# Kernel tuning notes

Hardware: AMD Instinct MI355X
Metric: run time of the kernel (lower is better)

## Reference

```python
import jax, jax.numpy as jnp
import numpy as np

DIM = 100
SAMPLE = 12
NEG = -9e15
LRELU = 0.2  # opt.alpha


def _forward(emb, pos_table, w1, w2, glu1_w, glu2_w, glu2_b,
             a0, a1, a2, a3, gw1, gw2, gw3, num_w, mask_item,
             alias_inputs, adj, items, seq_features, adj_all):
    B, L = items.shape
    h = emb[items]  # [B, L, D]

    # ---- LocalAggregator: e_k[b,i,j] = leaky_relu(sum_d h[b,i,d]*h[b,j,d]*a_k[d])
    # (same math as tiling to [B, N*N, D] then matmul with a_k, without the huge intermediate)
    def rel(a):
        return jax.nn.leaky_relu(jnp.einsum('bid,bjd->bij', h, h * a[:, 0]), LRELU)

    alpha = jnp.full((B, L, L), NEG, dtype=h.dtype)
    for k, a in enumerate((a0, a1, a2, a3)):
        alpha = jnp.where(adj == k + 1, rel(a), alpha)
    alpha = jax.nn.softmax(alpha, axis=-1)
    h_local = jnp.einsum('bij,bjd->bid', alpha, h)

    # ---- Global: sample 1-hop neighbors from adj_all / num tables
    nbr_idx = adj_all[items]          # [B, L, S]
    nbr_w = num_w[items]              # [B, L, S]
    nbr_vec = emb[nbr_idx]            # [B, L, S, D]

    # session info (mean of masked seq-feature embeddings)
    item_emb = emb[seq_features] * mask_item[..., None]
    sess = jnp.sum(item_emb, axis=1) / jnp.sum(mask_item, axis=-1, keepdims=True)  # [B, D]
    sess = jnp.broadcast_to(sess[:, None, :], (B, L, DIM))

    # GlobalAggregator with extra_vector
    a_in = jnp.concatenate([sess[:, :, None, :] * nbr_vec, nbr_w[..., None]], axis=-1)  # [B,L,S,D+1]
    att = jax.nn.leaky_relu(a_in @ gw1, LRELU)          # [B, L, S, D]
    att = jax.nn.softmax((att @ gw2)[..., 0], axis=-1)  # [B, L, S]
    agg = jnp.sum(att[..., None] * nbr_vec, axis=-2)    # [B, L, D]
    h_global = jax.nn.relu(jnp.concatenate([h, agg], axis=-1) @ gw3)

    h_comb = h_local + h_global
    seq_hidden = jnp.take_along_axis(h_comb, alias_inputs[..., None], axis=1)  # [B, L, D]

    rmask = mask_item[..., None]
    pos = jnp.broadcast_to(pos_table[:L][None], seq_hidden.shape)
    hs = jnp.sum(seq_hidden * rmask, axis=1) / jnp.sum(rmask, axis=1)  # [B, D]
    nh = jnp.tanh(jnp.concatenate([pos, seq_hidden], axis=-1) @ w1)
    nh = jax.nn.sigmoid(nh @ glu1_w + (hs @ glu2_w + glu2_b)[:, None, :])
    beta = (nh @ w2) * rmask                 # [B, L, 1]
    select = jnp.sum(beta * seq_hidden, 1)   # [B, D]
    score = select @ emb[1:].T               # skip item id 0 (padding)
    return jax.nn.softmax(score, axis=-1)


def setup_inputs():
    key = jax.random.key(0)
    B, L, NN, S, D = 256, 64, 100000, SAMPLE, DIM
    stdv = 1.0 / np.sqrt(D)
    ks = jax.random.split(key, 24)
    u = lambda k, s: jax.random.uniform(k, s, jnp.float32, -stdv, stdv)
    return {
        'emb': u(ks[0], (NN, D)),
        'pos_table': u(ks[1], (200, D)),
        'w1': u(ks[2], (2 * D, D)),
        'w2': u(ks[3], (D, 1)),
        'glu1_w': u(ks[4], (D, D)),
        'glu2_w': u(ks[5], (D, D)),
        'glu2_b': u(ks[6], (D,)),
        'a0': u(ks[7], (D, 1)),
        'a1': u(ks[8], (D, 1)),
        'a2': u(ks[9], (D, 1)),
        'a3': u(ks[10], (D, 1)),
        'gw1': u(ks[11], (D + 1, D)),
        'gw2': u(ks[12], (D, 1)),
        'gw3': u(ks[13], (2 * D, D)),
        'num_w': jax.random.uniform(ks[14], (NN, S), jnp.float32, 0.0, 1.0),
        'mask_item': jnp.ones((B, L), jnp.float32),
        'alias_inputs': jax.random.randint(ks[15], (B, L), 0, L),
        'adj': jax.random.randint(ks[16], (B, L, L), 0, 5),
        'items': jax.random.randint(ks[17], (B, L), 0, NN),
        'seq_features': jax.random.randint(ks[18], (B, L), 0, NN),
        'adj_all': jax.random.randint(ks[19], (NN, S), 0, NN),
    }


def reference(emb, pos_table, w1, w2, glu1_w, glu2_w, glu2_b, a0, a1, a2, a3,
              gw1, gw2, gw3, num_w, mask_item, alias_inputs, adj, items,
              seq_features, adj_all):
    return _forward(emb, pos_table, w1, w2, glu1_w, glu2_w, glu2_b,
                    a0, a1, a2, a3, gw1, gw2, gw3, num_w, mask_item,
                    alias_inputs, adj, items, seq_features, adj_all)
```

## Files before the change

kernel.cpp:

```cpp
#include <hip/hip_runtime.h>
#include <math.h>

#define B 256
#define L 64
#define D 100
#define S 12
#define NN 100000
#define E 99999
#define NEG -9e15f
#define LRELU 0.2f
#define M3A (B*L*S)
#define NT5 782

__device__ __forceinline__ float lrelu(float x){ return x > 0.f ? x : LRELU*x; }

__global__ void k0_pos(const float* __restrict__ pos, const float* __restrict__ w1,
                       float* __restrict__ pos_part){
    int l = blockIdx.x; int d = threadIdx.x;
    if (d >= D) return;
    float acc = 0.f;
    for (int c = 0; c < D; ++c) acc += pos[l*D+c] * w1[c*D+d];
    pos_part[l*D+d] = acc;
}

__global__ void k1_gather(const float* __restrict__ emb, const int* __restrict__ items,
                          const int* __restrict__ seqf, const float* __restrict__ mask,
                          float* __restrict__ h, float* __restrict__ sess){
    int b = blockIdx.x; int tid = threadIdx.x;
    for (int t = tid; t < L*D; t += blockDim.x){
        int l = t / D, d = t % D;
        h[(b*L+l)*D + d] = emb[(long)items[b*L+l]*D + d];
    }
    if (tid < D){
        float acc = 0.f, msum = 0.f;
        for (int l = 0; l < L; ++l){
            float mk = mask[b*L+l];
            acc  += emb[(long)seqf[b*L+l]*D + tid] * mk;
            msum += mk;
        }
        sess[b*D+tid] = acc / msum;
    }
}

__global__ __launch_bounds__(256) void k2_local(const float* __restrict__ h,
                         const int* __restrict__ adj,
                         const float* __restrict__ a0, const float* __restrict__ a1,
                         const float* __restrict__ a2, const float* __restrict__ a3,
                         float* __restrict__ hcomb){
    __shared__ __align__(16) float Hd[L*132];
    __shared__ float Alr[L*66];
    __shared__ __align__(16) float a4s[D*4];
    int tid = threadIdx.x;
    int tx = tid & 15, ty = tid >> 4;
    int b = blockIdx.x;

    for (int t = tid; t < D; t += 256){
        a4s[t*4+0] = a0[t]; a4s[t*4+1] = a1[t]; a4s[t*4+2] = a2[t]; a4s[t*4+3] = a3[t];
    }
    for (int e = tid; e < L*D; e += 256){
        int i = e / D, d = e - i*D;
        Hd[i*132 + d] = h[(long)(b*L+i)*D + d];
    }
    for (int e = tid; e < L*32; e += 256){
        int i = e >> 5, c = D + (e & 31);
        Hd[i*132 + c] = 0.f;
    }
    __syncthreads();

    int ksel[4][4];
    #pragma unroll
    for (int i=0;i<4;++i)
        #pragma unroll
        for (int j=0;j<4;++j)
            ksel[i][j] = adj[((long)b*L + ty*4+i)*L + tx*4+j];

    float e0[4][4]={}, e1[4][4]={}, e2[4][4]={}, e3[4][4]={};
    for (int d = 0; d < D; ++d){
        float4 aw = *(const float4*)&a4s[d*4];
        float hi[4], hj[4];
        #pragma unroll
        for (int i=0;i<4;++i) hi[i] = Hd[(ty*4+i)*132 + d];
        #pragma unroll
        for (int j=0;j<4;++j) hj[j] = Hd[(tx*4+j)*132 + d];
        #pragma unroll
        for (int i=0;i<4;++i)
            #pragma unroll
            for (int j=0;j<4;++j){
                float p = hi[i]*hj[j];
                e0[i][j] += p*aw.x;
                e1[i][j] += p*aw.y;
                e2[i][j] += p*aw.z;
                e3[i][j] += p*aw.w;
            }
    }

    #pragma unroll
    for (int i=0;i<4;++i){
        float s[4];
        #pragma unroll
        for (int j=0;j<4;++j){
            int k = ksel[i][j];
            float ev = (k==1) ? e0[i][j] : (k==2) ? e1[i][j]
                     : (k==3) ? e2[i][j] : e3[i][j];
            s[j] = (k>=1 && k<=4) ? lrelu(ev) : NEG;
        }
        float m = fmaxf(fmaxf(s[0],s[1]), fmaxf(s[2],s[3]));
        #pragma unroll
        for (int off=1; off<16; off<<=1) m = fmaxf(m, __shfl_xor(m, off));
        float es[4], sum = 0.f;
        #pragma unroll
        for (int j=0;j<4;++j){ es[j] = expf(s[j]-m); sum += es[j]; }
        #pragma unroll
        for (int off=1; off<16; off<<=1) sum += __shfl_xor(sum, off);
        float inv = 1.f/sum;
        #pragma unroll
        for (int j=0;j<4;++j) Alr[(ty*4+i)*66 + tx*4+j] = es[j]*inv;
    }
    __syncthreads();

    float o[4][8];
    #pragma unroll
    for (int i=0;i<4;++i)
        #pragma unroll
        for (int jj=0;jj<8;++jj) o[i][jj] = 0.f;
    for (int j = 0; j < L; ++j){
        float al[4];
        #pragma unroll
        for (int i=0;i<4;++i) al[i] = Alr[(ty*4+i)*66 + j];
        float4 b0 = *(const float4*)&Hd[j*132 + tx*4];
        float4 b1 = *(const float4*)&Hd[j*132 + 64 + tx*4];
        float bv[8] = {b0.x,b0.y,b0.z,b0.w,b1.x,b1.y,b1.z,b1.w};
        #pragma unroll
        for (int i=0;i<4;++i)
            #pragma unroll
            for (int jj=0;jj<8;++jj) o[i][jj] += al[i]*bv[jj];
    }
    #pragma unroll
    for (int i=0;i<4;++i){
        int row = ty*4+i;
        #pragma unroll
        for (int jj=0;jj<8;++jj){
            int d = (jj<4) ? (tx*4+jj) : (64 + tx*4 + (jj-4));
            if (d < D) hcomb[(long)(b*L+row)*D + d] = o[i][jj];
        }
    }
}

__global__ __launch_bounds__(256) void k3a_logits(const float* __restrict__ emb,
                          const float* __restrict__ sess,
                          const int* __restrict__ items, const int* __restrict__ adj_all,
                          const float* __restrict__ num_w,
                          const float* __restrict__ gw1, const float* __restrict__ gw2,
                          float* __restrict__ att_l){
    __shared__ __align__(16) float As[52*64];
    __shared__ __align__(16) float Bs[52*128];
    __shared__ float ss[104];
    __shared__ int   idxr[64];
    __shared__ float nbwr[64];
    __shared__ float gw2l[128];
    int tid = threadIdx.x;
    int tx = tid & 15, ty = tid >> 4;
    int r0 = blockIdx.x * 64;
    int b  = r0 / (L*S);

    if (tid < 64){
        int r = r0 + tid;
        int bl = r / S, s = r - bl*S;
        int it = items[bl];
        idxr[tid] = adj_all[it*S + s];
        nbwr[tid] = num_w[it*S + s];
    }
    if (tid < 104) ss[tid] = (tid < D) ? sess[b*D + tid] : 0.f;
    if (tid < 128) gw2l[tid] = (tid < D) ? gw2[tid] : 0.f;
    __syncthreads();

    float acc[4][8];
    #pragma unroll
    for (int i=0;i<4;++i)
        #pragma unroll
        for (int j=0;j<8;++j) acc[i][j] = 0.f;

    for (int chunk = 0; chunk < 2; ++chunk){
        int c0 = chunk*52;
        for (int e = tid; e < 64*13; e += 256){
            int rl = e & 63, cq = e >> 6;
            int cb = c0 + cq*4;
            float vx=0.f, vy=0.f, vz=0.f, vw=0.f;
            if (cb < D){
                const float4 v = *(const float4*)&emb[(long)idxr[rl]*D + cb];
                vx = v.x*ss[cb]; vy = v.y*ss[cb+1]; vz = v.z*ss[cb+2]; vw = v.w*ss[cb+3];
            } else if (cb == D){
                vx = nbwr[rl];
            }
            As[(cq*4+0)*64 + rl] = vx;
            As[(cq*4+1)*64 + rl] = vy;
            As[(cq*4+2)*64 + rl] = vz;
            As[(cq*4+3)*64 + rl] = vw;
        }
        for (int e = tid; e < 52*128; e += 256){
            int d = e & 127, cc = e >> 7;
            int c = c0 + cc;
            Bs[cc*128 + d] = (c <= D && d < D) ? gw1[c*D + d] : 0.f;
        }
        __syncthreads();
        for (int k = 0; k < 52; ++k){
            float4 a  = *(const float4*)&As[k*64 + ty*4];
            float4 b0 = *(const float4*)&Bs[k*128 + tx*4];
            float4 b1 = *(const float4*)&Bs[k*128 + 64 + tx*4];
            float av[4] = {a.x,a.y,a.z,a.w};
            float bv[8] = {b0.x,b0.y,b0.z,b0.w,b1.x,b1.y,b1.z,b1.w};
            #pragma unroll
            for (int i=0;i<4;++i)
                #pragma unroll
                for (int j=0;j<8;++j) acc[i][j] += av[i]*bv[j];
        }
        __syncthreads();
    }
    float g[8];
    #pragma unroll
    for (int j=0;j<8;++j) g[j] = gw2l[(j<4) ? (tx*4+j) : (64 + tx*4 + (j-4))];
    #pragma unroll
    for (int i=0;i<4;++i){
        float p = 0.f;
        #pragma unroll
        for (int j=0;j<8;++j) p += lrelu(acc[i][j]) * g[j];
        #pragma unroll
        for (int off=1; off<16; off<<=1) p += __shfl_xor(p, off);
        if (tx == 0) att_l[r0 + ty*4 + i] = p;
    }
}

__global__ __launch_bounds__(256) void k3b_agg(const float* __restrict__ emb,
                          const int* __restrict__ items, const int* __restrict__ adj_all,
                          const float* __restrict__ att_l,
                          float* __restrict__ agg){
    int p = blockIdx.x*2 + (threadIdx.x >> 7);
    int t = threadIdx.x & 127;
    float lg[S];
    float m = -INFINITY;
    #pragma unroll
    for (int s=0;s<S;++s){ lg[s] = att_l[p*S + s]; m = fmaxf(m, lg[s]); }
    float sum = 0.f;
    #pragma unroll
    for (int s=0;s<S;++s){ lg[s] = expf(lg[s]-m); sum += lg[s]; }
    float inv = 1.f/sum;
    if (t < D){
        int it = items[p];
        float acc = 0.f;
        #pragma unroll
        for (int s=0;s<S;++s){
            int idx = adj_all[it*S + s];
            acc += lg[s]*inv * emb[(long)idx*D + t];
        }
        agg[p*D + t] = acc;
    }
}

__global__ __launch_bounds__(256) void k3c_hg(const float* __restrict__ h,
                          const float* __restrict__ agg, const float* __restrict__ gw3,
                          float* __restrict__ hcomb){
    __shared__ __align__(16) float As[52*64];
    __shared__ __align__(16) float Bs[52*128];
    int tid = threadIdx.x;
    int tx = tid & 15, ty = tid >> 4;
    int r0 = blockIdx.x * 64;

    float acc[4][8];
    #pragma unroll
    for (int i=0;i<4;++i)
        #pragma unroll
        for (int j=0;j<8;++j) acc[i][j] = 0.f;

    for (int chunk = 0; chunk < 4; ++chunk){
        int c0 = chunk*52;
        for (int e = tid; e < 64*13; e += 256){
            int rl = e & 63, cq = e >> 6;
            int cb = c0 + cq*4;
            float4 v = {0.f,0.f,0.f,0.f};
            if (cb < D)            v = *(const float4*)&h[(long)(r0+rl)*D + cb];
            else if (cb < 2*D)     v = *(const float4*)&agg[(long)(r0+rl)*D + (cb-D)];
            As[(cq*4+0)*64 + rl] = v.x;
            As[(cq*4+1)*64 + rl] = v.y;
            As[(cq*4+2)*64 + rl] = v.z;
            As[(cq*4+3)*64 + rl] = v.w;
        }
        for (int e = tid; e < 52*128; e += 256){
            int d = e & 127, cc = e >> 7;
            int c = c0 + cc;
            Bs[cc*128 + d] = (c < 2*D && d < D) ? gw3[c*D + d] : 0.f;
        }
        __syncthreads();
        for (int k = 0; k < 52; ++k){
            float4 a  = *(const float4*)&As[k*64 + ty*4];
            float4 b0 = *(const float4*)&Bs[k*128 + tx*4];
            float4 b1 = *(const float4*)&Bs[k*128 + 64 + tx*4];
            float av[4] = {a.x,a.y,a.z,a.w};
            float bv[8] = {b0.x,b0.y,b0.z,b0.w,b1.x,b1.y,b1.z,b1.w};
            #pragma unroll
            for (int i=0;i<4;++i)
                #pragma unroll
                for (int j=0;j<8;++j) acc[i][j] += av[i]*bv[j];
        }
        __syncthreads();
    }
    #pragma unroll
    for (int i=0;i<4;++i){
        int r = r0 + ty*4 + i;
        #pragma unroll
        for (int j=0;j<8;++j){
            int d = (j<4) ? (tx*4+j) : (64 + tx*4 + (j-4));
            if (d < D){
                long o = (long)r*D + d;
                hcomb[o] += fmaxf(acc[i][j], 0.f);
            }
        }
    }
}

__global__ __launch_bounds__(128) void k4a_gate(const float* __restrict__ hcomb,
                          const int* __restrict__ alias_in, const float* __restrict__ mask,
                          const float* __restrict__ glu2_w, const float* __restrict__ glu2_b,
                          float* __restrict__ gate){
    int b = blockIdx.x; int tid = threadIdx.x;
    __shared__ float hsl[D];
    __shared__ float mkl[L];
    __shared__ int   al[L];
    if (tid < L){ al[tid] = alias_in[b*L+tid]; mkl[tid] = mask[b*L+tid]; }
    __syncthreads();
    if (tid < D){
        float acc = 0.f, msum = 0.f;
        for (int l = 0; l < L; ++l){
            acc  += hcomb[(long)(b*L + al[l])*D + tid] * mkl[l];
            msum += mkl[l];
        }
        hsl[tid] = acc / msum;
    }
    __syncthreads();
    if (tid < D){
        float g = glu2_b[tid];
        for (int c = 0; c < D; ++c) g += hsl[c]*glu2_w[c*D+tid];
        gate[b*D+tid] = g;
    }
}

__global__ __launch_bounds__(256) void k4b_nh1(const float* __restrict__ hcomb,
                          const int* __restrict__ alias_in,
                          const float* __restrict__ w1, const float* __restrict__ pos_part,
                          float* __restrict__ nh1){
    __shared__ __align__(16) float As[52*64];
    __shared__ __align__(16) float Bs[52*128];
    __shared__ int al[64];
    int tid = threadIdx.x;
    int tx = tid & 15, ty = tid >> 4;
    int b = blockIdx.x;
    int r0 = b * 64;

    if (tid < 64) al[tid] = alias_in[r0 + tid];
    __syncthreads();

    float acc[4][8];
    #pragma unroll
    for (int i=0;i<4;++i)
        #pragma unroll
        for (int j=0;j<8;++j) acc[i][j] = 0.f;

    for (int chunk = 0; chunk < 2; ++chunk){
        int c0 = chunk*52;
        for (int e = tid; e < 64*13; e += 256){
            int rl = e & 63, cq = e >> 6;
            int cb = c0 + cq*4;
            float4 v = {0.f,0.f,0.f,0.f};
            if (cb < D) v = *(const float4*)&hcomb[(long)(r0 + al[rl])*D + cb];
            As[(cq*4+0)*64 + rl] = v.x;
            As[(cq*4+1)*64 + rl] = v.y;
            As[(cq*4+2)*64 + rl] = v.z;
            As[(cq*4+3)*64 + rl] = v.w;
        }
        for (int e = tid; e < 52*128; e += 256){
            int d = e & 127, cc = e >> 7;
            int c = c0 + cc;
            Bs[cc*128 + d] = (c < D && d < D) ? w1[(D+c)*D + d] : 0.f;
        }
        __syncthreads();
        for (int k = 0; k < 52; ++k){
            float4 a  = *(const float4*)&As[k*64 + ty*4];
            float4 b0 = *(const float4*)&Bs[k*128 + tx*4];
            float4 b1 = *(const float4*)&Bs[k*128 + 64 + tx*4];
            float av[4] = {a.x,a.y,a.z,a.w};
            float bv[8] = {b0.x,b0.y,b0.z,b0.w,b1.x,b1.y,b1.z,b1.w};
            #pragma unroll
            for (int i=0;i<4;++i)
                #pragma unroll
                for (int j=0;j<8;++j) acc[i][j] += av[i]*bv[j];
        }
        __syncthreads();
    }
    #pragma unroll
    for (int i=0;i<4;++i){
        int rl = ty*4 + i;
        #pragma unroll
        for (int j=0;j<8;++j){
            int d = (j<4) ? (tx*4+j) : (64 + tx*4 + (j-4));
            if (d < D){
                float v = tanhf(acc[i][j] + pos_part[rl*D + d]);
                nh1[(long)(r0+rl)*D + d] = v;
            }
        }
    }
}

__global__ __launch_bounds__(256) void k4c_select(const float* __restrict__ nh1,
                          const float* __restrict__ hcomb, const int* __restrict__ alias_in,
                          const float* __restrict__ glu1_w, const float* __restrict__ gate,
                          const float* __restrict__ w2, const float* __restrict__ mask,
                          float* __restrict__ sel_out){
    __shared__ __align__(16) float As[104*64];
    __shared__ __align__(16) float Bs[52*128];
    __shared__ __align__(16) float Ss[64*D];
    __shared__ float red[16*128];
    __shared__ float w2l[128];
    __shared__ float mkl[64];
    __shared__ int   al[64];
    int tid = threadIdx.x;
    int tx = tid & 15, ty = tid >> 4;
    int b = blockIdx.x;
    int r0 = b * 64;

    if (tid < 64){ al[tid] = alias_in[r0 + tid]; mkl[tid] = mask[r0 + tid]; }
    if (tid < 128) w2l[tid] = (tid < D) ? w2[tid] : 0.f;
    __syncthreads();

    for (int e = tid; e < 64*26; e += 256){
        int rl = e & 63, cq = e >> 6;
        int cb = cq*4;
        float4 v = {0.f,0.f,0.f,0.f};
        if (cb < D) v = *(const float4*)&nh1[(long)(r0+rl)*D + cb];
        As[(cb+0)*64 + rl] = v.x;
        As[(cb+1)*64 + rl] = v.y;
        As[(cb+2)*64 + rl] = v.z;
        As[(cb+3)*64 + rl] = v.w;
    }
    for (int e = tid; e < 64*25; e += 256){
        int rl = e / 25, q = e % 25;
        *(float4*)&Ss[rl*D + q*4] = *(const float4*)&hcomb[(long)(r0 + al[rl])*D + q*4];
    }

    float acc[4][8];
    #pragma unroll
    for (int i=0;i<4;++i)
        #pragma unroll
        for (int j=0;j<8;++j) acc[i][j] = 0.f;

    for (int chunk = 0; chunk < 2; ++chunk){
        int c0 = chunk*52;
        __syncthreads();
        for (int e = tid; e < 52*128; e += 256){
            int d = e & 127, cc = e >> 7;
            int c = c0 + cc;
            Bs[cc*128 + d] = (c < D && d < D) ? glu1_w[c*D + d] : 0.f;
        }
        __syncthreads();
        for (int k = 0; k < 52; ++k){
            float4 a  = *(const float4*)&As[(c0+k)*64 + ty*4];
            float4 b0 = *(const float4*)&Bs[k*128 + tx*4];
            float4 b1 = *(const float4*)&Bs[k*128 + 64 + tx*4];
            float av[4] = {a.x,a.y,a.z,a.w};
            float bv[8] = {b0.x,b0.y,b0.z,b0.w,b1.x,b1.y,b1.z,b1.w};
            #pragma unroll
            for (int i=0;i<4;++i)
                #pragma unroll
                for (int j=0;j<8;++j) acc[i][j] += av[i]*bv[j];
        }
    }
    __syncthreads();

    float gl[8];
    #pragma unroll
    for (int j=0;j<8;++j){
        int d = (j<4) ? (tx*4+j) : (64 + tx*4 + (j-4));
        gl[j] = (d < D) ? gate[b*D + d] : 0.f;
    }
    float sp[8];
    #pragma unroll
    for (int j=0;j<8;++j) sp[j] = 0.f;
    #pragma unroll
    for (int i=0;i<4;++i){
        int rl = ty*4 + i;
        float p = 0.f;
        #pragma unroll
        for (int j=0;j<8;++j){
            int d = (j<4) ? (tx*4+j) : (64 + tx*4 + (j-4));
            float z = acc[i][j] + gl[j];
            float nh2 = 1.f/(1.f+expf(-z));
            p += nh2 * w2l[d];
        }
        #pragma unroll
        for (int off=1; off<16; off<<=1) p += __shfl_xor(p, off);
        float beta = p * mkl[rl];
        #pragma unroll
        for (int j=0;j<8;++j){
            int d = (j<4) ? (tx*4+j) : (64 + tx*4 + (j-4));
            if (d < D) sp[j] += beta * Ss[rl*D + d];
        }
    }
    #pragma unroll
    for (int j=0;j<8;++j){
        int d = (j<4) ? (tx*4+j) : (64 + tx*4 + (j-4));
        red[ty*128 + d] = sp[j];
    }
    __syncthreads();
    if (tid < 128){
        float s = 0.f;
        #pragma unroll
        for (int g=0; g<16; ++g) s += red[g*128 + tid];
        if (tid < D) sel_out[b*D + tid] = s;
    }
}

__global__ __launch_bounds__(256) void k5_score(const float* __restrict__ emb,
                                                const float* __restrict__ sel,
                                                float* __restrict__ out,
                                                float* __restrict__ pstats){
    __shared__ __align__(16) float As[52*64];
    __shared__ __align__(16) float Bs[52*128];
    int tid = threadIdx.x;
    int tx = tid & 15, ty = tid >> 4;
    int n0 = blockIdx.x * 128;
    int m0 = blockIdx.y * 64;

    float acc[4][8];
    #pragma unroll
    for (int i=0;i<4;++i)
        #pragma unroll
        for (int j=0;j<8;++j) acc[i][j] = 0.f;

    for (int chunk = 0; chunk < 2; ++chunk){
        int c0 = chunk*52;
        for (int e = tid; e < 64*13; e += 256){
            int rl = e & 63, cq = e >> 6;
            int cb = c0 + cq*4;
            float4 v = {0.f,0.f,0.f,0.f};
            if (cb < D) v = *(const float4*)&sel[(long)(m0+rl)*D + cb];
            As[(cq*4+0)*64 + rl] = v.x;
            As[(cq*4+1)*64 + rl] = v.y;
            As[(cq*4+2)*64 + rl] = v.z;
            As[(cq*4+3)*64 + rl] = v.w;
        }
        for (int e = tid; e < 128*13; e += 256){
            int nl = e & 127, cq = e >> 7;
            int cb = c0 + cq*4;
            int n = n0 + nl;
            float4 v = {0.f,0.f,0.f,0.f};
            if (cb < D && n < E) v = *(const float4*)&emb[(long)(1+n)*D + cb];
            Bs[(cq*4+0)*128 + nl] = v.x;
            Bs[(cq*4+1)*128 + nl] = v.y;
            Bs[(cq*4+2)*128 + nl] = v.z;
            Bs[(cq*4+3)*128 + nl] = v.w;
        }
        __syncthreads();
        for (int k = 0; k < 52; ++k){
            float4 a  = *(const float4*)&As[k*64 + ty*4];
            float4 b0 = *(const float4*)&Bs[k*128 + tx*4];
            float4 b1 = *(const float4*)&Bs[k*128 + 64 + tx*4];
            float av[4] = {a.x,a.y,a.z,a.w};
            float bv[8] = {b0.x,b0.y,b0.z,b0.w,b1.x,b1.y,b1.z,b1.w};
            #pragma unroll
            for (int i=0;i<4;++i)
                #pragma unroll
                for (int j=0;j<8;++j) acc[i][j] += av[i]*bv[j];
        }
        __syncthreads();
    }
    bool fullTile = (n0 + 128 <= E);
    #pragma unroll
    for (int i=0;i<4;++i){
        int m = m0 + ty*4 + i;
        long rowo = (long)m*E;
        if (fullTile){
            *(float4*)&out[rowo + n0 + tx*4]      = *(float4*)&acc[i][0];
            *(float4*)&out[rowo + n0 + 64 + tx*4] = *(float4*)&acc[i][4];
        } else {
            #pragma unroll
            for (int j=0;j<8;++j){
                int n = n0 + ((j<4) ? (tx*4+j) : (64 + tx*4 + (j-4)));
                if (n < E) out[rowo + n] = acc[i][j];
            }
        }
        float mx = -INFINITY, sm = 0.f;
        #pragma unroll
        for (int j=0;j<8;++j){
            int n = n0 + ((j<4) ? (tx*4+j) : (64 + tx*4 + (j-4)));
            if (n < E){
                float v = acc[i][j];
                if (v > mx){ sm = sm*expf(mx - v) + 1.f; mx = v; }
                else         sm += expf(v - mx);
            }
        }
        #pragma unroll
        for (int off=1; off<16; off<<=1){
            float mo = __shfl_xor(mx, off);
            float so = __shfl_xor(sm, off);
            float mm = fmaxf(mx, mo);
            float sn = 0.f;
            if (mx > -INFINITY) sn += sm*expf(mx-mm);
            if (mo > -INFINITY) sn += so*expf(mo-mm);
            mx = mm; sm = sn;
        }
        if (tx == 0){
            long o = ((long)m*NT5 + blockIdx.x)*2;
            pstats[o] = mx; pstats[o+1] = sm;
        }
    }
}

__global__ __launch_bounds__(256) void k7_combine(const float* __restrict__ pstats,
                                                  float* __restrict__ MS){
    int row = blockIdx.x;
    int tid = threadIdx.x;
    float m = -INFINITY, s = 0.f;
    for (int t = tid; t < NT5; t += 256){
        long o = ((long)row*NT5 + t)*2;
        float m2 = pstats[o], s2 = pstats[o+1];
        float mm = fmaxf(m, m2);
        float sn = 0.f;
        if (m  > -INFINITY) sn += s *expf(m -mm);
        if (m2 > -INFINITY) sn += s2*expf(m2-mm);
        m = mm; s = sn;
    }
    __shared__ float ms[256], ss[256];
    ms[tid] = m; ss[tid] = s;
    __syncthreads();
    for (int off = 128; off >= 1; off >>= 1){
        if (tid < off){
            float m1 = ms[tid], s1 = ss[tid];
            float m2 = ms[tid+off], s2 = ss[tid+off];
            float mm = fmaxf(m1, m2);
            float sn = 0.f;
            if (m1 > -INFINITY) sn += s1*expf(m1-mm);
            if (m2 > -INFINITY) sn += s2*expf(m2-mm);
            ms[tid] = mm; ss[tid] = sn;
        }
        __syncthreads();
    }
    if (tid == 0){ MS[row*2] = ms[0]; MS[row*2+1] = 1.f/ss[0]; }
}

__global__ __launch_bounds__(256) void k8_norm(float* __restrict__ out,
                                               const float* __restrict__ MS){
    int b = blockIdx.y;
    int n = blockIdx.x*256 + threadIdx.x;
    if (n < E){
        float m = MS[b*2], invs = MS[b*2+1];
        long i = (long)b*E + n;
        out[i] = expf(out[i] - m) * invs;
    }
}

extern "C" void kernel_launch(void* const* d_in, const int* in_sizes, int n_in,
                              void* d_out, int out_size, void* d_ws, size_t ws_size,
                              hipStream_t stream) {
    const float* emb       = (const float*)d_in[0];
    const float* pos_table = (const float*)d_in[1];
    const float* w1        = (const float*)d_in[2];
    const float* w2        = (const float*)d_in[3];
    const float* glu1_w    = (const float*)d_in[4];
    const float* glu2_w    = (const float*)d_in[5];
    const float* glu2_b    = (const float*)d_in[6];
    const float* a0        = (const float*)d_in[7];
    const float* a1        = (const float*)d_in[8];
    const float* a2        = (const float*)d_in[9];
    const float* a3        = (const float*)d_in[10];
    const float* gw1       = (const float*)d_in[11];
    const float* gw2       = (const float*)d_in[12];
    const float* gw3       = (const float*)d_in[13];
    const float* num_w     = (const float*)d_in[14];
    const float* mask      = (const float*)d_in[15];
    const int*   alias_in  = (const int*)d_in[16];
    const int*   adj       = (const int*)d_in[17];
    const int*   items     = (const int*)d_in[18];
    const int*   seqf      = (const int*)d_in[19];
    const int*   adj_all   = (const int*)d_in[20];

    float* ws       = (float*)d_ws;
    float* h        = ws;
    float* hcomb    = h + B*L*D;
    float* sess     = hcomb + B*L*D;
    float* pos_part = sess + B*D;
    float* sel      = pos_part + L*D;
    float* att_l    = sel + B*D;
    float* agg      = att_l + M3A;
    float* pstats   = agg + B*L*D;
    float* MS       = pstats + B*NT5*2;
    float* gate     = MS + B*2;
    float* nh1      = agg;

    float* out = (float*)d_out;

    k0_pos    <<<dim3(L), dim3(128), 0, stream>>>(pos_table, w1, pos_part);
    k1_gather <<<dim3(B), dim3(128), 0, stream>>>(emb, items, seqf, mask, h, sess);
    k2_local  <<<dim3(B), dim3(256), 0, stream>>>(h, adj, a0, a1, a2, a3, hcomb);
    k3a_logits<<<dim3(M3A/64), dim3(256), 0, stream>>>(emb, sess, items, adj_all, num_w,
                                                       gw1, gw2, att_l);
    k3b_agg   <<<dim3(B*L/2), dim3(256), 0, stream>>>(emb, items, adj_all, att_l, agg);
    k3c_hg    <<<dim3(B*L/64), dim3(256), 0, stream>>>(h, agg, gw3, hcomb);
    k4a_gate  <<<dim3(B), dim3(128), 0, stream>>>(hcomb, alias_in, mask, glu2_w, glu2_b, gate);
    k4b_nh1   <<<dim3(B), dim3(256), 0, stream>>>(hcomb, alias_in, w1, pos_part, nh1);
    k4c_select<<<dim3(B), dim3(256), 0, stream>>>(nh1, hcomb, alias_in, glu1_w, gate,
                                                  w2, mask, sel);
    k5_score  <<<dim3(NT5, 4), dim3(256), 0, stream>>>(emb, sel, out, pstats);
    k7_combine<<<dim3(B), dim3(256), 0, stream>>>(pstats, MS);
    k8_norm   <<<dim3((E + 255)/256, B), dim3(256), 0, stream>>>(out, MS);
}
```

Measured before the change: 665.9 us.

## Enlarge GEMM row tiles to 128 and vectorize gather and normalize kernels

The score GEMM and the neighbor-logit GEMM now compute 128-row tiles with an 8x8 per-thread accumulator instead of 64-row tiles. This halves the number of times the embedding table and gw1 are re-read from memory. The embedding gather in k1 and the softmax normalization in k8 now use float4 loads and stores, and k8 runs over a flat 1D grid. In exchange, register pressure and shared memory per block rise, which may lower occupancy, and k3a now reloads items, adj_all and sess from global memory inside its staging loop.

Result: faster. 642.8 us (-3.5%).

```diff
diff --git a/kernel.cpp b/kernel.cpp
--- a/kernel.cpp
+++ b/kernel.cpp
@@ -27,9 +27,10 @@
                           const int* __restrict__ seqf, const float* __restrict__ mask,
                           float* __restrict__ h, float* __restrict__ sess){
     int b = blockIdx.x; int tid = threadIdx.x;
-    for (int t = tid; t < L*D; t += blockDim.x){
-        int l = t / D, d = t % D;
-        h[(b*L+l)*D + d] = emb[(long)items[b*L+l]*D + d];
+    for (int e = tid; e < L*25; e += blockDim.x){
+        int l = e / 25, q = e % 25;
+        *(float4*)&h[(long)(b*L+l)*D + q*4] =
+            *(const float4*)&emb[(long)items[b*L+l]*D + q*4];
     }
     if (tid < D){
         float acc = 0.f, msum = 0.f;
@@ -152,50 +153,40 @@
                           const float* __restrict__ num_w,
                           const float* __restrict__ gw1, const float* __restrict__ gw2,
                           float* __restrict__ att_l){
-    __shared__ __align__(16) float As[52*64];
+    __shared__ __align__(16) float As[52*128];
     __shared__ __align__(16) float Bs[52*128];
-    __shared__ float ss[104];
-    __shared__ int   idxr[64];
-    __shared__ float nbwr[64];
-    __shared__ float gw2l[128];
     int tid = threadIdx.x;
     int tx = tid & 15, ty = tid >> 4;
-    int r0 = blockIdx.x * 64;
+    int r0 = blockIdx.x * 128;
     int b  = r0 / (L*S);
 
-    if (tid < 64){
-        int r = r0 + tid;
-        int bl = r / S, s = r - bl*S;
-        int it = items[bl];
-        idxr[tid] = adj_all[it*S + s];
-        nbwr[tid] = num_w[it*S + s];
-    }
-    if (tid < 104) ss[tid] = (tid < D) ? sess[b*D + tid] : 0.f;
-    if (tid < 128) gw2l[tid] = (tid < D) ? gw2[tid] : 0.f;
-    __syncthreads();
-
-    float acc[4][8];
-    #pragma unroll
-    for (int i=0;i<4;++i)
+    float acc[8][8];
+    #pragma unroll
+    for (int i=0;i<8;++i)
         #pragma unroll
         for (int j=0;j<8;++j) acc[i][j] = 0.f;
 
     for (int chunk = 0; chunk < 2; ++chunk){
         int c0 = chunk*52;
-        for (int e = tid; e < 64*13; e += 256){
-            int rl = e & 63, cq = e >> 6;
+        for (int e = tid; e < 128*13; e += 256){
+            int rl = e & 127, cq = e >> 7;
             int cb = c0 + cq*4;
+            int r = r0 + rl;
+            int bl = r / S, s = r - bl*S;
+            int it = items[bl];
             float vx=0.f, vy=0.f, vz=0.f, vw=0.f;
             if (cb < D){
-                const float4 v = *(const float4*)&emb[(long)idxr[rl]*D + cb];
-                vx = v.x*ss[cb]; vy = v.y*ss[cb+1]; vz = v.z*ss[cb+2]; vw = v.w*ss[cb+3];
+                int idx = adj_all[it*S + s];
+                const float4 v  = *(const float4*)&emb[(long)idx*D + cb];
+                const float4 sv = *(const float4*)&sess[(long)b*D + cb];
+                vx = v.x*sv.x; vy = v.y*sv.y; vz = v.z*sv.z; vw = v.w*sv.w;
             } else if (cb == D){
-                vx = nbwr[rl];
+                vx = num_w[it*S + s];
             }
-            As[(cq*4+0)*64 + rl] = vx;
-            As[(cq*4+1)*64 + rl] = vy;
-            As[(cq*4+2)*64 + rl] = vz;
-            As[(cq*4+3)*64 + rl] = vw;
+            As[(cq*4+0)*128 + rl] = vx;
+            As[(cq*4+1)*128 + rl] = vy;
+            As[(cq*4+2)*128 + rl] = vz;
+            As[(cq*4+3)*128 + rl] = vw;
         }
         for (int e = tid; e < 52*128; e += 256){
             int d = e & 127, cc = e >> 7;
@@ -204,13 +195,14 @@
         }
         __syncthreads();
         for (int k = 0; k < 52; ++k){
-            float4 a  = *(const float4*)&As[k*64 + ty*4];
+            float4 a0v = *(const float4*)&As[k*128 + ty*8];
+            float4 a1v = *(const float4*)&As[k*128 + ty*8 + 4];
             float4 b0 = *(const float4*)&Bs[k*128 + tx*4];
             float4 b1 = *(const float4*)&Bs[k*128 + 64 + tx*4];
-            float av[4] = {a.x,a.y,a.z,a.w};
+            float av[8] = {a0v.x,a0v.y,a0v.z,a0v.w,a1v.x,a1v.y,a1v.z,a1v.w};
             float bv[8] = {b0.x,b0.y,b0.z,b0.w,b1.x,b1.y,b1.z,b1.w};
             #pragma unroll
-            for (int i=0;i<4;++i)
+            for (int i=0;i<8;++i)
                 #pragma unroll
                 for (int j=0;j<8;++j) acc[i][j] += av[i]*bv[j];
         }
@@ -218,15 +210,18 @@
     }
     float g[8];
     #pragma unroll
-    for (int j=0;j<8;++j) g[j] = gw2l[(j<4) ? (tx*4+j) : (64 + tx*4 + (j-4))];
-    #pragma unroll
-    for (int i=0;i<4;++i){
+    for (int j=0;j<8;++j){
+        int d = (j<4) ? (tx*4+j) : (64 + tx*4 + (j-4));
+        g[j] = (d < D) ? gw2[d] : 0.f;
+    }
+    #pragma unroll
+    for (int i=0;i<8;++i){
         float p = 0.f;
         #pragma unroll
         for (int j=0;j<8;++j) p += lrelu(acc[i][j]) * g[j];
         #pragma unroll
         for (int off=1; off<16; off<<=1) p += __shfl_xor(p, off);
-        if (tx == 0) att_l[r0 + ty*4 + i] = p;
+        if (tx == 0) att_l[r0 + ty*8 + i] = p;
     }
 }
 
@@ -521,30 +516,30 @@
                                                 const float* __restrict__ sel,
                                                 float* __restrict__ out,
                                                 float* __restrict__ pstats){
-    __shared__ __align__(16) float As[52*64];
+    __shared__ __align__(16) float As[52*128];
     __shared__ __align__(16) float Bs[52*128];
     int tid = threadIdx.x;
     int tx = tid & 15, ty = tid >> 4;
     int n0 = blockIdx.x * 128;
-    int m0 = blockIdx.y * 64;
-
-    float acc[4][8];
-    #pragma unroll
-    for (int i=0;i<4;++i)
+    int m0 = blockIdx.y * 128;
+
+    float acc[8][8];
+    #pragma unroll
+    for (int i=0;i<8;++i)
         #pragma unroll
         for (int j=0;j<8;++j) acc[i][j] = 0.f;
 
     for (int chunk = 0; chunk < 2; ++chunk){
         int c0 = chunk*52;
-        for (int e = tid; e < 64*13; e += 256){
-            int rl = e & 63, cq = e >> 6;
+        for (int e = tid; e < 128*13; e += 256){
+            int rl = e & 127, cq = e >> 7;
             int cb = c0 + cq*4;
             float4 v = {0.f,0.f,0.f,0.f};
             if (cb < D) v = *(const float4*)&sel[(long)(m0+rl)*D + cb];
-            As[(cq*4+0)*64 + rl] = v.x;
-            As[(cq*4+1)*64 + rl] = v.y;
-            As[(cq*4+2)*64 + rl] = v.z;
-            As[(cq*4+3)*64 + rl] = v.w;
+            As[(cq*4+0)*128 + rl] = v.x;
+            As[(cq*4+1)*128 + rl] = v.y;
+            As[(cq*4+2)*128 + rl] = v.z;
+            As[(cq*4+3)*128 + rl] = v.w;
         }
         for (int e = tid; e < 128*13; e += 256){
             int nl = e & 127, cq = e >> 7;
@@ -559,13 +554,14 @@
         }
         __syncthreads();
         for (int k = 0; k < 52; ++k){
-            float4 a  = *(const float4*)&As[k*64 + ty*4];
+            float4 a0v = *(const float4*)&As[k*128 + ty*8];
+            float4 a1v = *(const float4*)&As[k*128 + ty*8 + 4];
             float4 b0 = *(const float4*)&Bs[k*128 + tx*4];
             float4 b1 = *(const float4*)&Bs[k*128 + 64 + tx*4];
-            float av[4] = {a.x,a.y,a.z,a.w};
+            float av[8] = {a0v.x,a0v.y,a0v.z,a0v.w,a1v.x,a1v.y,a1v.z,a1v.w};
             float bv[8] = {b0.x,b0.y,b0.z,b0.w,b1.x,b1.y,b1.z,b1.w};
             #pragma unroll
-            for (int i=0;i<4;++i)
+            for (int i=0;i<8;++i)
                 #pragma unroll
                 for (int j=0;j<8;++j) acc[i][j] += av[i]*bv[j];
         }
@@ -573,8 +569,8 @@
     }
     bool fullTile = (n0 + 128 <= E);
     #pragma unroll
-    for (int i=0;i<4;++i){
-        int m = m0 + ty*4 + i;
+    for (int i=0;i<8;++i){
+        int m = m0 + ty*8 + i;
         long rowo = (long)m*E;
         if (fullTile){
             *(float4*)&out[rowo + n0 + tx*4]      = *(float4*)&acc[i][0];
@@ -647,12 +643,19 @@
 
 __global__ __launch_bounds__(256) void k8_norm(float* __restrict__ out,
                                                const float* __restrict__ MS){
-    int b = blockIdx.y;
-    int n = blockIdx.x*256 + threadIdx.x;
-    if (n < E){
-        float m = MS[b*2], invs = MS[b*2+1];
-        long i = (long)b*E + n;
-        out[i] = expf(out[i] - m) * invs;
+    long base = ((long)blockIdx.x*256 + threadIdx.x)*4;
+    const long total = (long)B*E;
+    if (base < total){
+        float4 v = *(float4*)&out[base];
+        float r[4] = {v.x, v.y, v.z, v.w};
+        #pragma unroll
+        for (int c=0;c<4;++c){
+            long el = base + c;
+            int b = (int)(el / E);
+            r[c] = expf(r[c] - MS[b*2]) * MS[b*2+1];
+        }
+        v.x = r[0]; v.y = r[1]; v.z = r[2]; v.w = r[3];
+        *(float4*)&out[base] = v;
     }
 }
 
@@ -699,15 +702,15 @@
     k0_pos    <<<dim3(L), dim3(128), 0, stream>>>(pos_table, w1, pos_part);
     k1_gather <<<dim3(B), dim3(128), 0, stream>>>(emb, items, seqf, mask, h, sess);
     k2_local  <<<dim3(B), dim3(256), 0, stream>>>(h, adj, a0, a1, a2, a3, hcomb);
-    k3a_logits<<<dim3(M3A/64), dim3(256), 0, stream>>>(emb, sess, items, adj_all, num_w,
-                                                       gw1, gw2, att_l);
+    k3a_logits<<<dim3(M3A/128), dim3(256), 0, stream>>>(emb, sess, items, adj_all, num_w,
+                                                        gw1, gw2, att_l);
     k3b_agg   <<<dim3(B*L/2), dim3(256), 0, stream>>>(emb, items, adj_all, att_l, agg);
     k3c_hg    <<<dim3(B*L/64), dim3(256), 0, stream>>>(h, agg, gw3, hcomb);
     k4a_gate  <<<dim3(B), dim3(128), 0, stream>>>(hcomb, alias_in, mask, glu2_w, glu2_b, gate);
     k4b_nh1   <<<dim3(B), dim3(256), 0, stream>>>(hcomb, alias_in, w1, pos_part, nh1);
     k4c_select<<<dim3(B), dim3(256), 0, stream>>>(nh1, hcomb, alias_in, glu1_w, gate,
                                                   w2, mask, sel);
-    k5_score  <<<dim3(NT5, 4), dim3(256), 0, stream>>>(emb, sel, out, pstats);
+    k5_score  <<<dim3(NT5, 2), dim3(256), 0, stream>>>(emb, sel, out, pstats);
     k7_combine<<<dim3(B), dim3(256), 0, stream>>>(pstats, MS);
-    k8_norm   <<<dim3((E + 255)/256, B), dim3(256), 0, stream>>>(out, MS);
-}
+    k8_norm   <<<dim3((B*E/4 + 255)/256, 1), dim3(256), 0, stream>>>(out, MS);
+}
```
